# Performance work log

Measured on AMD Instinct MI355X. Metric: run time of the kernel, lower is better.

## Reference

```python
import jax, jax.numpy as jnp
import numpy as np

NUM_POINTS = 500_000
NUM_SUP = 8192
DEGREE = 32
HIDDEN = 256
NDIM = 3


def sincos_embed(coords, dim):
    # Faithful port of kappamodules ContinuousSincosEmbed.
    ndim = coords.shape[-1]
    ndim_padding = dim % ndim
    dim_per = (dim - ndim_padding) // ndim
    sincos_padding = dim_per % 2
    padding = ndim_padding + sincos_padding * ndim
    eff = (dim - padding) // ndim  # even
    omega = 1.0 / (10000.0 ** (jnp.arange(0, eff, 2, dtype=jnp.float32) / eff))
    out = coords[..., None] * omega  # (N, ndim, eff//2)
    emb = jnp.concatenate([jnp.sin(out), jnp.cos(out)], axis=-1)  # (N, ndim, eff)
    emb = emb.reshape(coords.shape[:-1] + (ndim * eff,))
    if padding > 0:
        emb = jnp.pad(emb, [(0, 0)] * (emb.ndim - 1) + [(0, padding)])
    return emb


def setup_inputs() -> dict:
    key = jax.random.key(0)
    ks = jax.random.split(key, 8)
    input_pos = jax.random.uniform(ks[0], (NUM_POINTS, NDIM), dtype=jnp.float32)
    supernode_idx = jnp.sort(
        jax.random.randint(ks[1], (NUM_SUP,), 0, NUM_POINTS, dtype=jnp.int32)
    )
    src_idx = jax.random.randint(ks[2], (NUM_SUP * DEGREE,), 0, NUM_POINTS, dtype=jnp.int32)
    dst_seg = jnp.repeat(jnp.arange(NUM_SUP, dtype=jnp.int32), DEGREE)
    s = 1.0 / np.sqrt(HIDDEN)
    w1 = jax.random.normal(ks[3], (HIDDEN, HIDDEN), dtype=jnp.float32) * s
    w2 = jax.random.normal(ks[4], (HIDDEN, HIDDEN), dtype=jnp.float32) * s
    wp = jax.random.normal(ks[5], (2 * HIDDEN, HIDDEN), dtype=jnp.float32) / np.sqrt(2 * HIDDEN)
    b1 = jnp.zeros((HIDDEN,), jnp.float32)
    b2 = jnp.zeros((HIDDEN,), jnp.float32)
    bp = jnp.zeros((HIDDEN,), jnp.float32)
    return {
        "input_pos": input_pos, "supernode_idx": supernode_idx,
        "src_idx": src_idx, "dst_seg": dst_seg,
        "w1": w1, "b1": b1, "w2": w2, "b2": b2, "wp": wp, "bp": bp,
    }


def reference(input_pos, supernode_idx, src_idx, dst_seg, w1, b1, w2, b2, wp, bp):
    num_sup = supernode_idx.shape[0]
    sup_pos = input_pos[supernode_idx]            # (S, 3)
    src_pos = input_pos[src_idx]                  # (E, 3)
    dst_pos = sup_pos[dst_seg]                    # (E, 3)
    dist = dst_pos - src_pos
    mag = jnp.linalg.norm(dist, axis=1, keepdims=True)
    rel = jnp.concatenate([dist, mag], axis=1)    # (E, 4)
    x = sincos_embed(rel, HIDDEN)                 # (E, H) relpos embed, ndim=4
    # message MLP: Linear -> GELU(exact) -> Linear
    x = jax.nn.gelu(x @ w1 + b1, approximate=False) @ w2 + b2
    # segment mean into supernodes (dst is sorted/consecutive per supernode)
    sums = jax.ops.segment_sum(x, dst_seg, num_segments=num_sup)
    counts = jax.ops.segment_sum(jnp.ones((x.shape[0],), x.dtype), dst_seg, num_segments=num_sup)
    agg = sums / jnp.maximum(counts, 1.0)[:, None]  # (S, H)
    sup_embed = sincos_embed(sup_pos, HIDDEN)       # (S, H) abspos embed, ndim=3
    out = jnp.concatenate([agg, sup_embed], axis=-1) @ wp + bp  # (S, H)
    return out[None]  # (1, S, H) -- batch_size=1 (batch_idx=None)
```

## Files before the change

kernel.cpp:

```cpp
#include <hip/hip_runtime.h>
#include <hip/hip_bf16.h>

typedef __bf16 bf16_t;
typedef bf16_t bf16x8 __attribute__((ext_vector_type(8)));
typedef float f32x16 __attribute__((ext_vector_type(16)));
typedef float f32x2 __attribute__((ext_vector_type(2)));

constexpr float OMG[16] = {
    1.0f,        0.74989421f, 0.56234133f, 0.42169650f,
    0.31622777f, 0.23713737f, 0.17782794f, 0.13335214f,
    0.1f,        0.074989421f, 0.056234133f, 0.042169650f,
    0.031622777f, 0.023713737f, 0.017782794f, 0.013335214f};

__device__ __forceinline__ f32x16 mfma_bf16(bf16x8 a, bf16x8 b, f32x16 c) {
  return __builtin_amdgcn_mfma_f32_32x32x16_bf16(a, b, c, 0, 0, 0);
}

__device__ __forceinline__ int orig_k(int pk) {
  return 64 * (pk >> 5) + 32 * ((pk >> 4) & 1) + (pk & 15);
}

__global__ __launch_bounds__(256) void prep(
    const float* __restrict__ w1, const float* __restrict__ b1,
    bf16_t* __restrict__ w1img, float* __restrict__ b1fold,
    f32x2* __restrict__ ometab, int* __restrict__ dtab) {
  __shared__ float T[256][33];
  const int bid = blockIdx.x;
  const int tid = threadIdx.x;

  if (bid < 8) {
    const int n0 = bid * 32;
#pragma unroll
    for (int it = 0; it < 16; ++it) {
      const int pk = it * 8 + (tid >> 5);
      T[pk][tid & 31] = w1[orig_k(pk) * 256 + n0 + (tid & 31)];
    }
    __syncthreads();
    const int n_off = tid & 31;
    const int n = n0 + n_off;
#pragma unroll
    for (int q = 0; q < 2; ++q) {
      const int slot = (tid >> 5) + 8 * q;
      bf16x8 v;
#pragma unroll
      for (int e = 0; e < 8; ++e) v[e] = (bf16_t)T[slot * 8 + e][n_off];
      *(bf16x8*)((char*)w1img + n * 256 + ((slot ^ (n & 15)) << 4)) = v;
    }
  } else if (bid == 8) {
    const int n = tid;
    float vl[4];
    float bf1 = b1[n];
#pragma unroll
    for (int d = 0; d < 4; ++d) {
      float s = 0.f;
#pragma unroll
      for (int i = 0; i < 16; ++i)
        s = fmaf(0.01f * OMG[i], w1[(64 * d + 16 + i) * 256 + n], s);
      vl[d] = s;
#pragma unroll
      for (int i = 0; i < 16; ++i) bf1 += w1[(64 * d + 48 + i) * 256 + n];
    }
    bf16_t* ext = w1img + 32768 + n * 16;
#pragma unroll
    for (int e = 0; e < 4; ++e) ext[e] = (bf16_t)vl[e];
#pragma unroll
    for (int e = 4; e < 16; ++e) ext[e] = (bf16_t)0.0f;
    b1fold[n] = bf1;
  } else {
    const int col = tid;
    float om = 0.0f, ph = 0.0f;
    int d = 0;
    if (col < 252) {
      d = (col >= 84 ? 1 : 0) + (col >= 168 ? 1 : 0);
      const int t3 = col - 84 * d;
      const int sc2 = (t3 >= 42) ? 1 : 0;
      om = __expf(-0.21929381838038533f * (float)(t3 - 42 * sc2));
      ph = sc2 ? 1.57079632679f : 0.0f;
    }
    f32x2 op; op[0] = om; op[1] = ph;
    ometab[col] = op;
    dtab[col] = d;
  }
}

#define AUX 88

__global__ __launch_bounds__(512, 2) void edge_mlp(
    const float* __restrict__ pos, const int* __restrict__ sup_idx,
    const int* __restrict__ src_idx,
    const bf16_t* __restrict__ w1img, const float* __restrict__ b1fold,
    const f32x2* __restrict__ ometab, const int* __restrict__ dtab,
    const float* __restrict__ w2, const float* __restrict__ wp,
    const float* __restrict__ b2, const float* __restrict__ bp,
    bf16_t* __restrict__ wpT2, float* __restrict__ bfold,
    bf16_t* __restrict__ cat) {
  __shared__ __attribute__((aligned(16))) char LDSbuf[73728];

  const int bid = blockIdx.x;
  const int tid = threadIdx.x;

  if (bid < 64) {
    const int o0 = (bid >> 3) * 32, j0 = (bid & 7) * 32;
    float* T = (float*)LDSbuf;
    {
      const int o_off = tid & 31;
      const int rr = tid >> 5;
#pragma unroll
      for (int it = 0; it < 16; ++it) {
        const int n = it * 16 + rr;
        T[n * 33 + o_off] = wp[n * 256 + o0 + o_off];
      }
    }
    __syncthreads();
    {
      const int o_off = tid & 31, jb = tid >> 5;
      float a0 = 0.f, a1 = 0.f;
      for (int n = 0; n < 256; ++n) {
        const float wv = T[n * 33 + o_off];
        a0 = fmaf(w2[(j0 + jb) * 256 + n], wv, a0);
        a1 = fmaf(w2[(j0 + jb + 16) * 256 + n], wv, a1);
      }
      wpT2[(o0 + o_off) * 512 + j0 + jb] = (bf16_t)a0;
      wpT2[(o0 + o_off) * 512 + j0 + jb + 16] = (bf16_t)a1;
    }
    return;
  } else if (bid < 72) {
    const int band = (bid - 64) * 32;
    float* T = (float*)LDSbuf;
    {
      const int o = tid & 255;
      const int ih = (tid >> 8) * 16;
#pragma unroll
      for (int it = 0; it < 16; ++it) {
        const int i = ih + it;
        T[o * 33 + i] = wp[(256 + band + i) * 256 + o];
      }
    }
    __syncthreads();
    {
      const int o = tid >> 1;
      const int gh = (tid & 1) * 2;
#pragma unroll
      for (int g = 0; g < 2; ++g) {
        const int gg = gh + g;
        bf16x8 v;
#pragma unroll
        for (int e = 0; e < 8; ++e) v[e] = (bf16_t)T[o * 33 + gg * 8 + e];
        *(bf16x8*)(wpT2 + o * 512 + 256 + band + gg * 8) = v;
      }
    }
    return;
  } else if (bid < AUX) {
    const int o = (bid - 72) * 16 + (tid >> 5);
    const int kl = (tid & 31) * 8;
    float s = 0.f;
#pragma unroll
    for (int k = 0; k < 8; ++k) s += b2[kl + k] * wp[(kl + k) * 256 + o];
    s += __shfl_xor(s, 16); s += __shfl_xor(s, 8); s += __shfl_xor(s, 4);
    s += __shfl_xor(s, 2); s += __shfl_xor(s, 1);
    if ((tid & 31) == 0) bfold[o] = s + bp[o];
    return;
  }

  bf16_t* Bs = (bf16_t*)LDSbuf;

  {
    const bf16x8* src8 = (const bf16x8*)w1img;
    bf16x8* dst8 = (bf16x8*)Bs;
#pragma unroll
    for (int it = 0; it < 9; ++it) {
      const int idx = it * 512 + tid;
      dst8[idx] = src8[idx];
    }
  }

  const int l = tid & 63, w = tid >> 6;
  const int hi = l >> 5, lc = l & 31;
  const int s = (bid - AUX) * 8 + w;

  const int si = sup_idx[s];
  const int srci = src_idx[s * 32 + lc];
  const float dx = pos[si * 3 + 0] - pos[srci * 3 + 0];
  const float dy = pos[si * 3 + 1] - pos[srci * 3 + 1];
  const float dz = pos[si * 3 + 2] - pos[srci * 3 + 2];
  const float mg = sqrtf(dx * dx + dy * dy + dz * dz);
  const float rv[4] = {dx, dy, dz, mg};

  float omg[8];
#pragma unroll
  for (int e = 0; e < 8; ++e) omg[e] = hi ? OMG[8 + e] : OMG[e];

  __syncthreads();

  f32x16 acc[8];
#pragma unroll
  for (int nt = 0; nt < 8; ++nt) {
    const float bi = b1fold[32 * nt + lc];
#pragma unroll
    for (int p = 0; p < 16; ++p) acc[nt][p] = bi;
  }

  const char* Bb = (const char*)Bs;

  {
    bf16x8 aext;
#pragma unroll
    for (int e = 0; e < 8; ++e)
      aext[e] = (hi == 0 && e < 4) ? (bf16_t)rv[e] : (bf16_t)0.0f;
    const char* eb = Bb + 65536 + lc * 32 + hi * 16;
#pragma unroll
    for (int nt = 0; nt < 8; ++nt) {
      bf16x8 be = *(const bf16x8*)(eb + nt * 1024);
      acc[nt] = mfma_bf16(aext, be, acc[nt]);
    }
  }

  const int sxor = (lc & 15) << 4;
  const int rowb = lc * 256;

#pragma unroll
  for (int d = 0; d < 4; ++d) {
    float ang[8];
#pragma unroll
    for (int e = 0; e < 8; ++e) ang[e] = rv[d] * omg[e];
    bf16x8 a_sin, a_cos;
#pragma unroll
    for (int e = 0; e < 8; ++e) a_sin[e] = (bf16_t)__sinf(ang[e]);
#pragma unroll
    for (int e = 0; e < 8; ++e) a_cos[e] = (bf16_t)__cosf(ang[e]);

    const int ko_sin = ((4 * d + hi) << 4) ^ sxor;
    const int ko_cos = ((4 * d + 2 + hi) << 4) ^ sxor;
#pragma unroll
    for (int g = 0; g < 2; ++g) {
      bf16x8 b0 = *(const bf16x8*)(Bb + rowb + (4 * g + 0) * 8192 + ko_sin);
      bf16x8 b1_ = *(const bf16x8*)(Bb + rowb + (4 * g + 1) * 8192 + ko_sin);
      bf16x8 b2_ = *(const bf16x8*)(Bb + rowb + (4 * g + 2) * 8192 + ko_sin);
      bf16x8 b3 = *(const bf16x8*)(Bb + rowb + (4 * g + 3) * 8192 + ko_sin);
      acc[4 * g + 0] = mfma_bf16(a_sin, b0, acc[4 * g + 0]);
      acc[4 * g + 1] = mfma_bf16(a_sin, b1_, acc[4 * g + 1]);
      acc[4 * g + 2] = mfma_bf16(a_sin, b2_, acc[4 * g + 2]);
      acc[4 * g + 3] = mfma_bf16(a_sin, b3, acc[4 * g + 3]);
    }
#pragma unroll
    for (int g = 0; g < 2; ++g) {
      bf16x8 b0 = *(const bf16x8*)(Bb + rowb + (4 * g + 0) * 8192 + ko_cos);
      bf16x8 b1_ = *(const bf16x8*)(Bb + rowb + (4 * g + 1) * 8192 + ko_cos);
      bf16x8 b2_ = *(const bf16x8*)(Bb + rowb + (4 * g + 2) * 8192 + ko_cos);
      bf16x8 b3 = *(const bf16x8*)(Bb + rowb + (4 * g + 3) * 8192 + ko_cos);
      acc[4 * g + 0] = mfma_bf16(a_cos, b0, acc[4 * g + 0]);
      acc[4 * g + 1] = mfma_bf16(a_cos, b1_, acc[4 * g + 1]);
      acc[4 * g + 2] = mfma_bf16(a_cos, b2_, acc[4 * g + 2]);
      acc[4 * g + 3] = mfma_bf16(a_cos, b3, acc[4 * g + 3]);
    }
  }

  const f32x2 C2v = {-0.10296644f, -0.10296644f};
  const f32x2 C0v = {-2.3022765f, -2.3022765f};
#pragma unroll
  for (int nt = 0; nt < 8; ++nt) {
    f32x2 ss2 = {0.0f, 0.0f};
#pragma unroll
    for (int p = 0; p < 16; p += 2) {
      f32x2 x; x[0] = acc[nt][p]; x[1] = acc[nt][p + 1];
      f32x2 u = x * x;
      f32x2 t = u * C2v + C0v;
      f32x2 v = x * t;
      f32x2 e; e[0] = exp2f(v[0]); e[1] = exp2f(v[1]);
      f32x2 den = e + 1.0f;
      f32x2 r;
      r[0] = __builtin_amdgcn_rcpf(den[0]);
      r[1] = __builtin_amdgcn_rcpf(den[1]);
      ss2 = x * r + ss2;
    }
    float ssum = ss2[0] + ss2[1];
    ssum += __shfl_xor(ssum, 32);
    if (hi == 0) cat[s * 512 + 32 * nt + lc] = (bf16_t)(ssum * 0.03125f);
  }

#pragma unroll
  for (int q = 0; q < 4; ++q) {
    const int col = 64 * q + l;
    const f32x2 op = ometab[col];
    const int d = dtab[col];
    const float pd = pos[si * 3 + d];
    const float v = __sinf(fmaf(pd, op[0], op[1]));
    cat[s * 512 + 256 + col] = (bf16_t)v;
  }
}

__global__ __launch_bounds__(256) void proj(
    const bf16_t* __restrict__ cat, const bf16_t* __restrict__ wpT2,
    const float* __restrict__ bfold, float* __restrict__ out) {
  const int tid = threadIdx.x;
  const int l = tid & 63, w = tid >> 6;
  const int hi = l >> 5, lc = l & 31;
  const int rm = blockIdx.x * 64;
  const int cn = blockIdx.y * 128 + w * 32;
  const int r0 = rm + lc, r1 = rm + 32 + lc;
  const int c0 = cn + lc;

  f32x16 a0, a1;
#pragma unroll
  for (int p = 0; p < 16; ++p) { a0[p] = 0.f; a1[p] = 0.f; }
#pragma unroll 8
  for (int kk = 0; kk < 32; ++kk) {
    int k0 = kk * 16 + 8 * hi;
    bf16x8 fa0 = *(const bf16x8*)(cat + r0 * 512 + k0);
    bf16x8 fa1 = *(const bf16x8*)(cat + r1 * 512 + k0);
    bf16x8 fb = *(const bf16x8*)(wpT2 + c0 * 512 + k0);
    a0 = mfma_bf16(fa0, fb, a0);
    a1 = mfma_bf16(fa1, fb, a1);
  }
  float bias = bfold[c0];
#pragma unroll
  for (int rr = 0; rr < 16; ++rr) {
    int rowo = (rr & 3) + 8 * (rr >> 2) + 4 * hi;
    out[(rm + rowo) * 256 + c0] = a0[rr] + bias;
    out[(rm + 32 + rowo) * 256 + c0] = a1[rr] + bias;
  }
}

extern "C" void kernel_launch(void* const* d_in, const int* in_sizes, int n_in,
                              void* d_out, int out_size, void* d_ws, size_t ws_size,
                              hipStream_t stream) {
  const float* pos = (const float*)d_in[0];
  const int* sup_idx = (const int*)d_in[1];
  const int* src_idx = (const int*)d_in[2];
  const float* w1 = (const float*)d_in[4];
  const float* b1 = (const float*)d_in[5];
  const float* w2 = (const float*)d_in[6];
  const float* b2 = (const float*)d_in[7];
  const float* wp = (const float*)d_in[8];
  const float* bp = (const float*)d_in[9];

  char* ws = (char*)d_ws;
  bf16_t* w1img  = (bf16_t*)(ws);
  bf16_t* wpT2   = (bf16_t*)(ws + 73728);
  float*  bfold  = (float*)(ws + 335872);
  float*  b1fold = (float*)(ws + 336896);
  f32x2*  ometab = (f32x2*)(ws + 337920);
  int*    dtab   = (int*)(ws + 339968);
  bf16_t* cat    = (bf16_t*)(ws + 340992);
  float* out = (float*)d_out;

  if (ws_size < (size_t)(340992 + 8192 * 512 * 2)) return;

  prep<<<dim3(10), dim3(256), 0, stream>>>(w1, b1, w1img, b1fold, ometab, dtab);
  edge_mlp<<<dim3(AUX + 1024), dim3(512), 0, stream>>>(
      pos, sup_idx, src_idx, w1img, b1fold, ometab, dtab,
      w2, wp, b2, bp, wpT2, bfold, cat);
  proj<<<dim3(128, 2), dim3(256), 0, stream>>>(cat, wpT2, bfold, out);
}
```

Before: 69.63 us.

## Compute folded W2·Wp weight product with MFMA and move aux blocks after edge blocks

The folded weight product (w2 times the top half of wp, written transposed into wpT2) was computed by 64 scalar-FMA blocks. Now prep converts w2 and transposes wp's top half to bf16, and two MFMA blocks compute the product. The auxiliary blocks are placed after the 1024 edge blocks instead of before them, so edge work starts immediately and the aux blocks shrink from 88 to 12. The bias fold is also reorganised. In exchange, prep launches more blocks and the fold is computed from bf16 inputs, which loses some precision.

```diff
diff --git a/kernel.cpp b/kernel.cpp
--- a/kernel.cpp
+++ b/kernel.cpp
@@ -22,8 +22,10 @@
 
 __global__ __launch_bounds__(256) void prep(
     const float* __restrict__ w1, const float* __restrict__ b1,
+    const float* __restrict__ w2, const float* __restrict__ wp,
     bf16_t* __restrict__ w1img, float* __restrict__ b1fold,
-    f32x2* __restrict__ ometab, int* __restrict__ dtab) {
+    f32x2* __restrict__ ometab, int* __restrict__ dtab,
+    bf16_t* __restrict__ wpTa, bf16_t* __restrict__ w2b) {
   __shared__ float T[256][33];
   const int bid = blockIdx.x;
   const int tid = threadIdx.x;
@@ -66,7 +68,7 @@
 #pragma unroll
     for (int e = 4; e < 16; ++e) ext[e] = (bf16_t)0.0f;
     b1fold[n] = bf1;
-  } else {
+  } else if (bid == 9) {
     const int col = tid;
     float om = 0.0f, ph = 0.0f;
     int d = 0;
@@ -80,18 +82,40 @@
     f32x2 op; op[0] = om; op[1] = ph;
     ometab[col] = op;
     dtab[col] = d;
-  }
-}
-
-#define AUX 88
+  } else if (bid < 18) {
+    const int band = (bid - 10) * 32;
+#pragma unroll
+    for (int it = 0; it < 32; ++it)
+      T[tid][it] = wp[(band + it) * 256 + tid];
+    __syncthreads();
+    const int o = tid;
+#pragma unroll
+    for (int g = 0; g < 4; ++g) {
+      bf16x8 v;
+#pragma unroll
+      for (int e = 0; e < 8; ++e) v[e] = (bf16_t)T[o][g * 8 + e];
+      *(bf16x8*)(wpTa + o * 256 + band + g * 8) = v;
+    }
+  } else {
+    const int base = (bid - 18) * 8192;
+#pragma unroll
+    for (int it = 0; it < 32; ++it) {
+      const int idx = base + it * 256 + tid;
+      w2b[idx] = (bf16_t)w2[idx];
+    }
+  }
+}
+
+#define NEDGE 1024
 
 __global__ __launch_bounds__(512, 2) void edge_mlp(
     const float* __restrict__ pos, const int* __restrict__ sup_idx,
     const int* __restrict__ src_idx,
     const bf16_t* __restrict__ w1img, const float* __restrict__ b1fold,
     const f32x2* __restrict__ ometab, const int* __restrict__ dtab,
-    const float* __restrict__ w2, const float* __restrict__ wp,
-    const float* __restrict__ b2, const float* __restrict__ bp,
+    const bf16_t* __restrict__ wpTa, const bf16_t* __restrict__ w2b,
+    const float* __restrict__ wp, const float* __restrict__ b2,
+    const float* __restrict__ bp,
     bf16_t* __restrict__ wpT2, float* __restrict__ bfold,
     bf16_t* __restrict__ cat) {
   __shared__ __attribute__((aligned(16))) char LDSbuf[73728];
@@ -99,66 +123,74 @@
   const int bid = blockIdx.x;
   const int tid = threadIdx.x;
 
-  if (bid < 64) {
-    const int o0 = (bid >> 3) * 32, j0 = (bid & 7) * 32;
-    float* T = (float*)LDSbuf;
-    {
-      const int o_off = tid & 31;
-      const int rr = tid >> 5;
-#pragma unroll
-      for (int it = 0; it < 16; ++it) {
-        const int n = it * 16 + rr;
-        T[n * 33 + o_off] = wp[n * 256 + o0 + o_off];
+  if (bid >= NEDGE) {
+    const int aux = bid - NEDGE;
+    if (aux < 2) {
+      const int l = tid & 63, w = tid >> 6;
+      const int wm = w >> 2, wn = w & 3;
+      const int rm = aux * 128 + wm * 64;
+      const int cn = wn * 64;
+      const int asel = l >> 5, lr = l & 31;
+      const int r0 = rm + lr, r1 = rm + 32 + lr;
+      const int c0 = cn + lr, c1 = cn + 32 + lr;
+      f32x16 a00, a01, a10, a11;
+#pragma unroll
+      for (int q = 0; q < 16; ++q) { a00[q] = 0.f; a01[q] = 0.f; a10[q] = 0.f; a11[q] = 0.f; }
+#pragma unroll 4
+      for (int kk = 0; kk < 16; ++kk) {
+        int k0 = kk * 16 + 8 * asel;
+        bf16x8 fa0 = *(const bf16x8*)(wpTa + r0 * 256 + k0);
+        bf16x8 fa1 = *(const bf16x8*)(wpTa + r1 * 256 + k0);
+        bf16x8 fb0 = *(const bf16x8*)(w2b + c0 * 256 + k0);
+        bf16x8 fb1 = *(const bf16x8*)(w2b + c1 * 256 + k0);
+        a00 = mfma_bf16(fa0, fb0, a00);
+        a01 = mfma_bf16(fa0, fb1, a01);
+        a10 = mfma_bf16(fa1, fb0, a10);
+        a11 = mfma_bf16(fa1, fb1, a11);
       }
-    }
-    __syncthreads();
-    {
-      const int o_off = tid & 31, jb = tid >> 5;
-      float a0 = 0.f, a1 = 0.f;
-      for (int n = 0; n < 256; ++n) {
-        const float wv = T[n * 33 + o_off];
-        a0 = fmaf(w2[(j0 + jb) * 256 + n], wv, a0);
-        a1 = fmaf(w2[(j0 + jb + 16) * 256 + n], wv, a1);
+#pragma unroll
+      for (int rr = 0; rr < 16; ++rr) {
+        int rowo = (rr & 3) + 8 * (rr >> 2) + 4 * asel;
+        wpT2[(rm + rowo) * 512 + c0] = (bf16_t)a00[rr];
+        wpT2[(rm + rowo) * 512 + c1] = (bf16_t)a01[rr];
+        wpT2[(rm + 32 + rowo) * 512 + c0] = (bf16_t)a10[rr];
+        wpT2[(rm + 32 + rowo) * 512 + c1] = (bf16_t)a11[rr];
       }
-      wpT2[(o0 + o_off) * 512 + j0 + jb] = (bf16_t)a0;
-      wpT2[(o0 + o_off) * 512 + j0 + jb + 16] = (bf16_t)a1;
-    }
-    return;
-  } else if (bid < 72) {
-    const int band = (bid - 64) * 32;
-    float* T = (float*)LDSbuf;
-    {
-      const int o = tid & 255;
-      const int ih = (tid >> 8) * 16;
-#pragma unroll
-      for (int it = 0; it < 16; ++it) {
-        const int i = ih + it;
-        T[o * 33 + i] = wp[(256 + band + i) * 256 + o];
+    } else if (aux < 10) {
+      const int band = (aux - 2) * 32;
+      float* T = (float*)LDSbuf;
+      {
+        const int o = tid & 255;
+        const int ih = (tid >> 8) * 16;
+#pragma unroll
+        for (int it = 0; it < 16; ++it) {
+          const int i = ih + it;
+          T[o * 33 + i] = wp[(256 + band + i) * 256 + o];
+        }
       }
-    }
-    __syncthreads();
-    {
-      const int o = tid >> 1;
-      const int gh = (tid & 1) * 2;
-#pragma unroll
-      for (int g = 0; g < 2; ++g) {
-        const int gg = gh + g;
-        bf16x8 v;
-#pragma unroll
-        for (int e = 0; e < 8; ++e) v[e] = (bf16_t)T[o * 33 + gg * 8 + e];
-        *(bf16x8*)(wpT2 + o * 512 + 256 + band + gg * 8) = v;
+      __syncthreads();
+      {
+        const int o = tid >> 1;
+        const int gh = (tid & 1) * 2;
+#pragma unroll
+        for (int g = 0; g < 2; ++g) {
+          const int gg = gh + g;
+          bf16x8 v;
+#pragma unroll
+          for (int e = 0; e < 8; ++e) v[e] = (bf16_t)T[o * 33 + gg * 8 + e];
+          *(bf16x8*)(wpT2 + o * 512 + 256 + band + gg * 8) = v;
+        }
       }
-    }
-    return;
-  } else if (bid < AUX) {
-    const int o = (bid - 72) * 16 + (tid >> 5);
-    const int kl = (tid & 31) * 8;
-    float s = 0.f;
-#pragma unroll
-    for (int k = 0; k < 8; ++k) s += b2[kl + k] * wp[(kl + k) * 256 + o];
-    s += __shfl_xor(s, 16); s += __shfl_xor(s, 8); s += __shfl_xor(s, 4);
-    s += __shfl_xor(s, 2); s += __shfl_xor(s, 1);
-    if ((tid & 31) == 0) bfold[o] = s + bp[o];
+    } else {
+      const int o = (aux - 10) * 128 + (tid >> 2);
+      const int kl = (tid & 3) * 64;
+      float s = 0.f;
+#pragma unroll 8
+      for (int i = 0; i < 64; ++i) s += b2[kl + i] * wp[(kl + i) * 256 + o];
+      s += __shfl_xor(s, 1);
+      s += __shfl_xor(s, 2);
+      if ((tid & 3) == 0) bfold[o] = s + bp[o];
+    }
     return;
   }
 
@@ -176,7 +208,7 @@
 
   const int l = tid & 63, w = tid >> 6;
   const int hi = l >> 5, lc = l & 31;
-  const int s = (bid - AUX) * 8 + w;
+  const int s = bid * 8 + w;
 
   const int si = sup_idx[s];
   const int srci = src_idx[s * 32 + lc];
@@ -341,14 +373,17 @@
   float*  b1fold = (float*)(ws + 336896);
   f32x2*  ometab = (f32x2*)(ws + 337920);
   int*    dtab   = (int*)(ws + 339968);
-  bf16_t* cat    = (bf16_t*)(ws + 340992);
+  bf16_t* wpTa   = (bf16_t*)(ws + 340992);
+  bf16_t* w2b    = (bf16_t*)(ws + 472064);
+  bf16_t* cat    = (bf16_t*)(ws + 603136);
   float* out = (float*)d_out;
 
-  if (ws_size < (size_t)(340992 + 8192 * 512 * 2)) return;
-
-  prep<<<dim3(10), dim3(256), 0, stream>>>(w1, b1, w1img, b1fold, ometab, dtab);
-  edge_mlp<<<dim3(AUX + 1024), dim3(512), 0, stream>>>(
+  if (ws_size < (size_t)(603136 + 8192 * 512 * 2)) return;
+
+  prep<<<dim3(26), dim3(256), 0, stream>>>(
+      w1, b1, w2, wp, w1img, b1fold, ometab, dtab, wpTa, w2b);
+  edge_mlp<<<dim3(NEDGE + 12), dim3(512), 0, stream>>>(
       pos, sup_idx, src_idx, w1img, b1fold, ometab, dtab,
-      w2, wp, b2, bp, wpT2, bfold, cat);
+      wpTa, w2b, wp, b2, bp, wpT2, bfold, cat);
   proj<<<dim3(128, 2), dim3(256), 0, stream>>>(cat, wpT2, bfold, out);
 }
```

Result: slower. 74.77 us (+7.4%).
